# Kernel tuning notes

Measured on AMD Instinct MI355X. Metric: run time of the kernel, lower is better.

The kernel has to match this reference:

```python
import jax, jax.numpy as jnp
import numpy as np

T, IN, H, OUT = 4096, 512, 2048, 4


def setup_inputs() -> dict:
    key = jax.random.key(0)
    ks = jax.random.split(key, 10)
    s_in = 1.0 / np.sqrt(IN)   # fan-in scaled init for input weights
    s_h = 1.0 / np.sqrt(H)     # fan-in scaled init for recurrent weights
    return {
        "x": jax.random.normal(ks[0], (T, IN), jnp.float32),
        "h0": jnp.zeros((H,), jnp.float32),
        "hebb0": jnp.zeros((H, H), jnp.float32),
        "Wz": jax.random.normal(ks[1], (IN, H), jnp.float32) * s_in,
        "Uz": jax.random.normal(ks[2], (H, H), jnp.float32) * s_h,
        "bz": jnp.zeros((H,), jnp.float32),
        "Wr": jax.random.normal(ks[3], (IN, H), jnp.float32) * s_in,
        "Ur": jax.random.normal(ks[4], (H, H), jnp.float32) * s_h,
        "br": jnp.zeros((H,), jnp.float32),
        "Wh": jax.random.normal(ks[5], (IN, H), jnp.float32) * s_in,
        "Uh": jax.random.normal(ks[6], (H, H), jnp.float32) * s_h,
        "bh": jnp.zeros((H,), jnp.float32),
        "alpha": jax.random.normal(ks[7], (H, H), jnp.float32) * 0.01,
        "eta": jnp.full((1,), 0.01, jnp.float32),
        "Wo": jax.random.normal(ks[8], (H, OUT), jnp.float32) * s_h,
        "bo": jnp.zeros((OUT,), jnp.float32),
        "seed": 0,
    }


def reference(x, h0, hebb0, Wz, Uz, bz, Wr, Ur, br, Wh, Uh, bh, alpha, eta, Wo, bo, seed):
    eta_s = eta[0]
    # Precompute all input-to-hidden projections in one batched GEMM (time-parallel).
    xz = x @ Wz + bz          # [T, H]
    xr = x @ Wr + br          # [T, H]
    xh = x @ Wh + bh          # [T, H]

    def step(carry, xt):
        h, hebb = carry                         # h: [H], hebb: [H, H]
        xzt, xrt, xht = xt
        z = jax.nn.sigmoid(xzt + h @ Uz)        # update gate
        r = jax.nn.sigmoid(xrt + h @ Ur)        # reset gate
        rh = r * h
        # plastic recurrent weight: Uh + alpha (elementwise) * hebb fast weights
        h_tilde = jnp.tanh(xht + rh @ Uh + rh @ (alpha * hebb))
        h_new = (1.0 - z) * h + z * h_tilde
        # Hebbian trace: decaying outer-product of pre/post activities
        hebb_new = (1.0 - eta_s) * hebb + eta_s * jnp.outer(h, h_new)
        return (h_new, hebb_new), h_new

    (hT, hebbT), y = jax.lax.scan(step, (h0, hebb0), (xz, xr, xh))  # y: [T, H]
    output = y @ Wo + bo                         # [T, OUT]
    act_rng = jax.random.fold_in(jax.random.key(seed), 1)
    action = jax.random.categorical(act_rng, output[:, :2])  # [T]
    return (output, action, hT, hebbT)
```

## Files before the change

### kernel.cpp

```cpp
#include <hip/hip_runtime.h>
#include <stdint.h>

#define T_STEPS 4096
#define IN_DIM  512
#define H_DIM   2048
#define NBLK    256
#define STH     512

typedef unsigned int uint32;

__device__ __forceinline__ double wredd(double v) {
#pragma unroll
  for (int m = 32; m >= 1; m >>= 1) v += __shfl_xor(v, m, 64);
  return v;
}

__device__ __forceinline__ double agloadd(const double* p) {
  return __hip_atomic_load(const_cast<double*>(p), __ATOMIC_RELAXED, __HIP_MEMORY_SCOPE_AGENT);
}
__device__ __forceinline__ void agstored(double* p, double v) {
  __hip_atomic_store(p, v, __ATOMIC_RELAXED, __HIP_MEMORY_SCOPE_AGENT);
}

__device__ __forceinline__ void threefry2x32(uint32 k0, uint32 k1, uint32& x0, uint32& x1) {
  uint32 ks2 = k0 ^ k1 ^ 0x1BD11BDAu;
  x0 += k0; x1 += k1;
#define TF_R(r) { x0 += x1; x1 = (x1 << r) | (x1 >> (32 - r)); x1 ^= x0; }
  TF_R(13) TF_R(15) TF_R(26) TF_R(6)
  x0 += k1;  x1 += ks2 + 1u;
  TF_R(17) TF_R(29) TF_R(16) TF_R(24)
  x0 += ks2; x1 += k0 + 2u;
  TF_R(13) TF_R(15) TF_R(26) TF_R(6)
  x0 += k0;  x1 += k1 + 3u;
  TF_R(17) TF_R(29) TF_R(16) TF_R(24)
  x0 += k1;  x1 += ks2 + 4u;
  TF_R(13) TF_R(15) TF_R(26) TF_R(6)
  x0 += ks2; x1 += k0 + 5u;
#undef TF_R
}

__global__ void __launch_bounds__(256) transpose_all(
    const float* __restrict__ Uz, const float* __restrict__ Ur,
    const float* __restrict__ Uh, const float* __restrict__ Al,
    const float* __restrict__ Wz, const float* __restrict__ Wr, const float* __restrict__ Wh,
    const float* __restrict__ Hb0,
    float* __restrict__ UZT, float* __restrict__ URT,
    float* __restrict__ UHT, float* __restrict__ AT,
    float* __restrict__ WZT, float* __restrict__ WRT, float* __restrict__ WHT,
    float* __restrict__ HBT) {
  __shared__ float sm[64][65];
  const float* in; float* out; int R, C;
  switch (blockIdx.z) {
    case 0: in = Uz;  out = UZT; R = H_DIM; C = H_DIM; break;
    case 1: in = Ur;  out = URT; R = H_DIM; C = H_DIM; break;
    case 2: in = Uh;  out = UHT; R = H_DIM; C = H_DIM; break;
    case 3: in = Al;  out = AT;  R = H_DIM; C = H_DIM; break;
    case 4: in = Hb0; out = HBT; R = H_DIM; C = H_DIM; break;
    case 5: in = Wz;  out = WZT; R = IN_DIM; C = H_DIM; break;
    case 6: in = Wr;  out = WRT; R = IN_DIM; C = H_DIM; break;
    default: in = Wh; out = WHT; R = IN_DIM; C = H_DIM; break;
  }
  int r0 = blockIdx.y * 64, c0 = blockIdx.x * 64;
  if (r0 >= R) return;
#pragma unroll
  for (int l = 0; l < 16; ++l) {
    int idx = threadIdx.x + l * 256;
    int r = idx >> 6, c = idx & 63;
    sm[r][c] = in[(size_t)(r0 + r) * C + c0 + c];
  }
  __syncthreads();
#pragma unroll
  for (int l = 0; l < 16; ++l) {
    int idx = threadIdx.x + l * 256;
    int r = idx >> 6, c = idx & 63;
    out[(size_t)(c0 + r) * R + r0 + c] = sm[c][r];
  }
}

__device__ __forceinline__ void gridbar(uint32* slots, uint32* go, int b, int tid, uint32 phase) {
  __syncthreads();
  if (b == 0) {
    if (tid > 0 && tid < NBLK) {
      while (__hip_atomic_load(&slots[tid * 16], __ATOMIC_ACQUIRE, __HIP_MEMORY_SCOPE_AGENT) < phase) {}
    }
    __syncthreads();
    if (tid == 0) {
      __hip_atomic_store(go, phase, __ATOMIC_RELEASE, __HIP_MEMORY_SCOPE_AGENT);
    }
  } else {
    if (tid == 0) {
      __hip_atomic_store(&slots[b * 16], phase, __ATOMIC_RELEASE, __HIP_MEMORY_SCOPE_AGENT);
      while (__hip_atomic_load(go, __ATOMIC_ACQUIRE, __HIP_MEMORY_SCOPE_AGENT) < phase) {}
    }
  }
  __syncthreads();
}

__global__ void __launch_bounds__(STH, 1) scan_kernel(
    const float* __restrict__ h0, const float* __restrict__ x,
    const float* __restrict__ bz, const float* __restrict__ br, const float* __restrict__ bh,
    const float* __restrict__ eta_p,
    const float* __restrict__ UZT, const float* __restrict__ URT,
    const float* __restrict__ UHT, const float* __restrict__ AT,
    const float* __restrict__ WZT, const float* __restrict__ WRT, const float* __restrict__ WHT,
    float* __restrict__ HBT,
    double* __restrict__ Y, double* __restrict__ RH,
    uint32* slots, uint32* go) {
  __shared__ double hbufA[H_DIM];
  __shared__ double hbufB[H_DIM];
  __shared__ double rhsh[H_DIM];
  __shared__ float  xsh[IN_DIM];
  const int b = blockIdx.x, tid = threadIdx.x;
  const int w = tid >> 6, lane = tid & 63;
  const int j0 = b * 8, j = j0 + w;
  const double eta = (double)eta_p[0], dec = 1.0 - eta;
  const double bzj = (double)bz[j], brj = (double)br[j], bhj = (double)bh[j];

  double hb[32];
  const float* hbtj = HBT + (size_t)j * H_DIM;
#pragma unroll
  for (int m = 0; m < 32; ++m) hb[m] = (double)hbtj[m * 64 + lane];

  const float* uzp = UZT + (size_t)j * H_DIM;
  const float* urp = URT + (size_t)j * H_DIM;
  const float* uhp = UHT + (size_t)j * H_DIM;
  const float* atp = AT  + (size_t)j * H_DIM;
  const float* wzp = WZT + (size_t)j * IN_DIM;
  const float* wrp = WRT + (size_t)j * IN_DIM;
  const float* whp = WHT + (size_t)j * IN_DIM;
  double* hcur = hbufA; double* hprv = hbufB;
  uint32 phase = 0;

  for (int t = 0; t < T_STEPS; ++t) {
    if (t == 0) {
      for (int k = tid; k < H_DIM; k += STH) hcur[k] = (double)h0[k];
    } else {
      const double* yp = Y + (size_t)(t - 1) * H_DIM;
      for (int k = tid; k < H_DIM; k += STH) hcur[k] = agloadd(yp + k);
    }
    for (int k = tid; k < IN_DIM; k += STH) xsh[k] = x[(size_t)t * IN_DIM + k];
    __syncthreads();

    double sz = 0.0, sr = 0.0, sh = 0.0;
#pragma unroll
    for (int m = 0; m < IN_DIM / 64; ++m) {
      int i = m * 64 + lane;
      double xv = (double)xsh[i];
      sz = fma(xv, (double)wzp[i], sz);
      sr = fma(xv, (double)wrp[i], sr);
      sh = fma(xv, (double)whp[i], sh);
    }
#pragma unroll 8
    for (int m = 0; m < H_DIM / 64; ++m) {
      int i = m * 64 + lane;
      double hv = hcur[i];
      sz = fma(hv, (double)uzp[i], sz);
      sr = fma(hv, (double)urp[i], sr);
    }
    sz = wredd(sz); sr = wredd(sr);
    double z = 1.0 / (1.0 + exp(-(sz + bzj)));
    double r = 1.0 / (1.0 + exp(-(sr + brj)));
    double hj = hcur[j];
    if (lane == 0) agstored(&RH[j], r * hj);

    ++phase; gridbar(slots, go, b, tid, phase);

    for (int k = tid; k < H_DIM; k += STH) rhsh[k] = agloadd(&RH[k]);
    __syncthreads();

    double acc = sh;
    if (t == 0) {
#pragma unroll
      for (int m = 0; m < 32; ++m) {
        int i = m * 64 + lane;
        acc = fma(rhsh[i], fma((double)atp[i], hb[m], (double)uhp[i]), acc);
      }
    } else {
      double cj = eta * hj;
#pragma unroll
      for (int m = 0; m < 32; ++m) {
        int i = m * 64 + lane;
        double hbv = fma(cj, hprv[i], dec * hb[m]);
        hb[m] = hbv;
        acc = fma(rhsh[i], fma((double)atp[i], hbv, (double)uhp[i]), acc);
      }
    }
    acc = wredd(acc);
    double htl = tanh(acc + bhj);
    double hnew = (1.0 - z) * hj + z * htl;
    if (lane == 0) agstored(&Y[(size_t)t * H_DIM + j], hnew);

    ++phase; gridbar(slots, go, b, tid, phase);

    double* tmp = hcur; hcur = hprv; hprv = tmp;
  }

  const double* hA = Y + (size_t)(T_STEPS - 2) * H_DIM;
  double hbj = agloadd(Y + (size_t)(T_STEPS - 1) * H_DIM + j);
  float* hbto = HBT + (size_t)j * H_DIM;
#pragma unroll
  for (int m = 0; m < 32; ++m) {
    int i = m * 64 + lane;
    hbto[i] = (float)fma(eta * agloadd(hA + i), hbj, dec * hb[m]);
  }
}

__global__ void __launch_bounds__(64) outk(
    const double* __restrict__ Y, const float* __restrict__ Wo,
    const float* __restrict__ bo, const int* __restrict__ seedp,
    float* __restrict__ out) {
  int bid = blockIdx.x, lane = threadIdx.x;
  if (bid >= T_STEPS) {
    int jj = (bid - T_STEPS) * 64 + lane;
    out[20480 + jj] = (float)Y[(size_t)(T_STEPS - 1) * H_DIM + jj];
    return;
  }
  int t = bid;
  double a0 = 0., a1 = 0., a2 = 0., a3 = 0.;
  const double* yrow = Y + (size_t)t * H_DIM;
  for (int jj = lane; jj < H_DIM; jj += 64) {
    double yv = yrow[jj];
    float4 wv = ((const float4*)Wo)[jj];
    a0 = fma(yv, (double)wv.x, a0); a1 = fma(yv, (double)wv.y, a1);
    a2 = fma(yv, (double)wv.z, a2); a3 = fma(yv, (double)wv.w, a3);
  }
  a0 = wredd(a0); a1 = wredd(a1); a2 = wredd(a2); a3 = wredd(a3);
  if (lane == 0) {
    double l0 = a0 + (double)bo[0], l1 = a1 + (double)bo[1];
    double l2 = a2 + (double)bo[2], l3 = a3 + (double)bo[3];
    float4 o; o.x = (float)l0; o.y = (float)l1; o.z = (float)l2; o.w = (float)l3;
    ((float4*)out)[t] = o;

    long long sv = (long long)seedp[0];
    uint32 k0 = (uint32)(((unsigned long long)sv) >> 32), k1 = (uint32)(sv & 0xffffffffLL);
    uint32 ak0 = 0u, ak1 = 1u;
    threefry2x32(k0, k1, ak0, ak1);
    uint32 p0 = 0u, p1 = (uint32)(2 * t);
    threefry2x32(ak0, ak1, p0, p1);
    uint32 b0 = p0 ^ p1;
    uint32 q0 = 0u, q1 = (uint32)(2 * t + 1);
    threefry2x32(ak0, ak1, q0, q1);
    uint32 b1 = q0 ^ q1;
    const float tiny = 1.1754943508222875e-38f;
    float f0 = __uint_as_float((b0 >> 9) | 0x3f800000u) - 1.0f;
    float f1 = __uint_as_float((b1 >> 9) | 0x3f800000u) - 1.0f;
    float u0 = fmaxf(tiny, fmaf(f0, 1.0f - tiny, tiny));
    float u1 = fmaxf(tiny, fmaf(f1, 1.0f - tiny, tiny));
    float g0 = -logf(-logf(u0));
    float g1 = -logf(-logf(u1));
    double s0 = l0 + (double)g0, s1 = l1 + (double)g1;
    out[16384 + t] = (s1 > s0) ? 1.0f : 0.0f;
  }
}

__global__ void __launch_bounds__(256) hebbout_kernel(const float* __restrict__ HBT,
                                                      float* __restrict__ out) {
  __shared__ float sm[64][65];
  int j0 = blockIdx.x * 64, i0 = blockIdx.y * 64;
#pragma unroll
  for (int l = 0; l < 16; ++l) {
    int idx = threadIdx.x + l * 256;
    int r = idx >> 6, c = idx & 63;
    sm[r][c] = HBT[(size_t)(j0 + r) * H_DIM + i0 + c];
  }
  __syncthreads();
#pragma unroll
  for (int l = 0; l < 16; ++l) {
    int idx = threadIdx.x + l * 256;
    int r = idx >> 6, c = idx & 63;
    out[22528 + (size_t)(i0 + r) * H_DIM + j0 + c] = sm[c][r];
  }
}

extern "C" void kernel_launch(void* const* d_in, const int* in_sizes, int n_in,
                              void* d_out, int out_size, void* d_ws, size_t ws_size,
                              hipStream_t stream) {
  (void)in_sizes; (void)n_in; (void)out_size; (void)ws_size;
  const float* x     = (const float*)d_in[0];
  const float* h0    = (const float*)d_in[1];
  const float* hebb0 = (const float*)d_in[2];
  const float* Wz    = (const float*)d_in[3];
  const float* Uz    = (const float*)d_in[4];
  const float* bz    = (const float*)d_in[5];
  const float* Wr    = (const float*)d_in[6];
  const float* Ur    = (const float*)d_in[7];
  const float* br    = (const float*)d_in[8];
  const float* Wh    = (const float*)d_in[9];
  const float* Uh    = (const float*)d_in[10];
  const float* bh    = (const float*)d_in[11];
  const float* alpha = (const float*)d_in[12];
  const float* eta   = (const float*)d_in[13];
  const float* Wo    = (const float*)d_in[14];
  const float* bo    = (const float*)d_in[15];
  const int*   seed  = (const int*)d_in[16];

  const size_t TH = (size_t)T_STEPS * H_DIM;
  const size_t HH = (size_t)H_DIM * H_DIM;
  const size_t HI = (size_t)H_DIM * IN_DIM;
  double* Y  = (double*)d_ws;
  double* RH = Y + TH;
  float* UZT = (float*)(RH + H_DIM);
  float* URT = UZT + HH;
  float* UHT = URT + HH;
  float* AT  = UHT + HH;
  float* WZT = AT + HH;
  float* WRT = WZT + HI;
  float* WHT = WRT + HI;
  float* HBT = WHT + HI;
  uint32* slots = (uint32*)(HBT + HH);
  uint32* go    = slots + NBLK * 16;

  hipMemsetAsync(slots, 0, (NBLK * 16 + 16) * sizeof(uint32), stream);
  transpose_all<<<dim3(32, 32, 8), 256, 0, stream>>>(Uz, Ur, Uh, alpha, Wz, Wr, Wh, hebb0,
                                                     UZT, URT, UHT, AT, WZT, WRT, WHT, HBT);
  float* out = (float*)d_out;
  scan_kernel<<<NBLK, STH, 0, stream>>>(h0, x, bz, br, bh, eta,
                                        UZT, URT, UHT, AT, WZT, WRT, WHT,
                                        HBT, Y, RH, slots, go);
  outk<<<T_STEPS + 32, 64, 0, stream>>>(Y, Wo, bo, seed, out);
  hebbout_kernel<<<dim3(32, 32), 256, 0, stream>>>(HBT, out);
}
```

Measured before the change: 352.0 ms.

## Replicate broadcast buffers, per-block go flags, float4 loads, early hebb update

```diff
diff --git a/kernel.cpp b/kernel.cpp
--- a/kernel.cpp
+++ b/kernel.cpp
@@ -6,6 +6,7 @@
 #define H_DIM   2048
 #define NBLK    256
 #define STH     512
+#define NREP    8
 
 typedef unsigned int uint32;
 
@@ -77,20 +78,20 @@
   }
 }
 
-__device__ __forceinline__ void gridbar(uint32* slots, uint32* go, int b, int tid, uint32 phase) {
+__device__ __forceinline__ void gridbar(uint32* slots, uint32* goarr, int b, int tid, uint32 phase) {
   __syncthreads();
   if (b == 0) {
-    if (tid > 0 && tid < NBLK) {
+    if (tid >= 1 && tid < NBLK) {
       while (__hip_atomic_load(&slots[tid * 16], __ATOMIC_ACQUIRE, __HIP_MEMORY_SCOPE_AGENT) < phase) {}
     }
     __syncthreads();
-    if (tid == 0) {
-      __hip_atomic_store(go, phase, __ATOMIC_RELEASE, __HIP_MEMORY_SCOPE_AGENT);
+    if (tid < NBLK) {
+      __hip_atomic_store(&goarr[tid * 16], phase, __ATOMIC_RELEASE, __HIP_MEMORY_SCOPE_AGENT);
     }
   } else {
     if (tid == 0) {
       __hip_atomic_store(&slots[b * 16], phase, __ATOMIC_RELEASE, __HIP_MEMORY_SCOPE_AGENT);
-      while (__hip_atomic_load(go, __ATOMIC_ACQUIRE, __HIP_MEMORY_SCOPE_AGENT) < phase) {}
+      while (__hip_atomic_load(&goarr[b * 16], __ATOMIC_ACQUIRE, __HIP_MEMORY_SCOPE_AGENT) < phase) {}
     }
   }
   __syncthreads();
@@ -104,104 +105,124 @@
     const float* __restrict__ UHT, const float* __restrict__ AT,
     const float* __restrict__ WZT, const float* __restrict__ WRT, const float* __restrict__ WHT,
     float* __restrict__ HBT,
-    double* __restrict__ Y, double* __restrict__ RH,
-    uint32* slots, uint32* go) {
-  __shared__ double hbufA[H_DIM];
-  __shared__ double hbufB[H_DIM];
+    double* __restrict__ Y, double* __restrict__ Hrep, double* __restrict__ RHrep,
+    uint32* slots, uint32* goarr) {
+  __shared__ double hcur[H_DIM];
   __shared__ double rhsh[H_DIM];
   __shared__ float  xsh[IN_DIM];
   const int b = blockIdx.x, tid = threadIdx.x;
   const int w = tid >> 6, lane = tid & 63;
-  const int j0 = b * 8, j = j0 + w;
+  const int j = b * 8 + w;
+  const int rep = b & (NREP - 1);
   const double eta = (double)eta_p[0], dec = 1.0 - eta;
   const double bzj = (double)bz[j], brj = (double)br[j], bhj = (double)bh[j];
 
   double hb[32];
-  const float* hbtj = HBT + (size_t)j * H_DIM;
-#pragma unroll
-  for (int m = 0; m < 32; ++m) hb[m] = (double)hbtj[m * 64 + lane];
-
-  const float* uzp = UZT + (size_t)j * H_DIM;
-  const float* urp = URT + (size_t)j * H_DIM;
-  const float* uhp = UHT + (size_t)j * H_DIM;
-  const float* atp = AT  + (size_t)j * H_DIM;
-  const float* wzp = WZT + (size_t)j * IN_DIM;
-  const float* wrp = WRT + (size_t)j * IN_DIM;
-  const float* whp = WHT + (size_t)j * IN_DIM;
-  double* hcur = hbufA; double* hprv = hbufB;
+  const float4* hbt4 = (const float4*)(HBT + (size_t)j * H_DIM);
+#pragma unroll
+  for (int m = 0; m < 8; ++m) {
+    float4 v = hbt4[m * 64 + lane];
+    hb[4 * m + 0] = (double)v.x; hb[4 * m + 1] = (double)v.y;
+    hb[4 * m + 2] = (double)v.z; hb[4 * m + 3] = (double)v.w;
+  }
+
+  const float4* uz4 = (const float4*)(UZT + (size_t)j * H_DIM);
+  const float4* ur4 = (const float4*)(URT + (size_t)j * H_DIM);
+  const float4* uh4 = (const float4*)(UHT + (size_t)j * H_DIM);
+  const float4* at4 = (const float4*)(AT  + (size_t)j * H_DIM);
+  const float4* wz4 = (const float4*)(WZT + (size_t)j * IN_DIM);
+  const float4* wr4 = (const float4*)(WRT + (size_t)j * IN_DIM);
+  const float4* wh4 = (const float4*)(WHT + (size_t)j * IN_DIM);
   uint32 phase = 0;
 
   for (int t = 0; t < T_STEPS; ++t) {
     if (t == 0) {
       for (int k = tid; k < H_DIM; k += STH) hcur[k] = (double)h0[k];
     } else {
-      const double* yp = Y + (size_t)(t - 1) * H_DIM;
-      for (int k = tid; k < H_DIM; k += STH) hcur[k] = agloadd(yp + k);
+      const double* hp = Hrep + (size_t)rep * H_DIM;
+      for (int k = tid; k < H_DIM; k += STH) hcur[k] = agloadd(hp + k);
     }
     for (int k = tid; k < IN_DIM; k += STH) xsh[k] = x[(size_t)t * IN_DIM + k];
     __syncthreads();
 
     double sz = 0.0, sr = 0.0, sh = 0.0;
-#pragma unroll
-    for (int m = 0; m < IN_DIM / 64; ++m) {
-      int i = m * 64 + lane;
-      double xv = (double)xsh[i];
-      sz = fma(xv, (double)wzp[i], sz);
-      sr = fma(xv, (double)wrp[i], sr);
-      sh = fma(xv, (double)whp[i], sh);
-    }
-#pragma unroll 8
-    for (int m = 0; m < H_DIM / 64; ++m) {
-      int i = m * 64 + lane;
-      double hv = hcur[i];
-      sz = fma(hv, (double)uzp[i], sz);
-      sr = fma(hv, (double)urp[i], sr);
+    const float4* x4 = (const float4*)xsh;
+#pragma unroll
+    for (int m = 0; m < IN_DIM / 256; ++m) {
+      int i4 = m * 64 + lane;
+      float4 xv = x4[i4], az = wz4[i4], ar = wr4[i4], ah = wh4[i4];
+      sz = fma((double)xv.x, (double)az.x, sz); sz = fma((double)xv.y, (double)az.y, sz);
+      sz = fma((double)xv.z, (double)az.z, sz); sz = fma((double)xv.w, (double)az.w, sz);
+      sr = fma((double)xv.x, (double)ar.x, sr); sr = fma((double)xv.y, (double)ar.y, sr);
+      sr = fma((double)xv.z, (double)ar.z, sr); sr = fma((double)xv.w, (double)ar.w, sr);
+      sh = fma((double)xv.x, (double)ah.x, sh); sh = fma((double)xv.y, (double)ah.y, sh);
+      sh = fma((double)xv.z, (double)ah.z, sh); sh = fma((double)xv.w, (double)ah.w, sh);
+    }
+    const double2* h2 = (const double2*)hcur;
+#pragma unroll
+    for (int m = 0; m < H_DIM / 256; ++m) {
+      int i4 = m * 64 + lane;
+      float4 az = uz4[i4], ar = ur4[i4];
+      double2 hA = h2[2 * i4], hB = h2[2 * i4 + 1];
+      sz = fma(hA.x, (double)az.x, sz); sz = fma(hA.y, (double)az.y, sz);
+      sz = fma(hB.x, (double)az.z, sz); sz = fma(hB.y, (double)az.w, sz);
+      sr = fma(hA.x, (double)ar.x, sr); sr = fma(hA.y, (double)ar.y, sr);
+      sr = fma(hB.x, (double)ar.z, sr); sr = fma(hB.y, (double)ar.w, sr);
     }
     sz = wredd(sz); sr = wredd(sr);
     double z = 1.0 / (1.0 + exp(-(sz + bzj)));
     double r = 1.0 / (1.0 + exp(-(sr + brj)));
     double hj = hcur[j];
-    if (lane == 0) agstored(&RH[j], r * hj);
-
-    ++phase; gridbar(slots, go, b, tid, phase);
-
-    for (int k = tid; k < H_DIM; k += STH) rhsh[k] = agloadd(&RH[k]);
+    double rhj = r * hj;
+    if (lane < NREP) agstored(&RHrep[(size_t)lane * H_DIM + j], rhj);
+
+    ++phase; gridbar(slots, goarr, b, tid, phase);
+
+    {
+      const double* rp = RHrep + (size_t)rep * H_DIM;
+      for (int k = tid; k < H_DIM; k += STH) rhsh[k] = agloadd(rp + k);
+    }
     __syncthreads();
 
     double acc = sh;
-    if (t == 0) {
-#pragma unroll
-      for (int m = 0; m < 32; ++m) {
-        int i = m * 64 + lane;
-        acc = fma(rhsh[i], fma((double)atp[i], hb[m], (double)uhp[i]), acc);
-      }
-    } else {
-      double cj = eta * hj;
-#pragma unroll
-      for (int m = 0; m < 32; ++m) {
-        int i = m * 64 + lane;
-        double hbv = fma(cj, hprv[i], dec * hb[m]);
-        hb[m] = hbv;
-        acc = fma(rhsh[i], fma((double)atp[i], hbv, (double)uhp[i]), acc);
-      }
+    const double2* r2 = (const double2*)rhsh;
+#pragma unroll
+    for (int m = 0; m < 8; ++m) {
+      int i4 = m * 64 + lane;
+      float4 av = at4[i4], uv = uh4[i4];
+      double2 rA = r2[2 * i4], rB = r2[2 * i4 + 1];
+      acc = fma(rA.x, fma((double)av.x, hb[4 * m + 0], (double)uv.x), acc);
+      acc = fma(rA.y, fma((double)av.y, hb[4 * m + 1], (double)uv.y), acc);
+      acc = fma(rB.x, fma((double)av.z, hb[4 * m + 2], (double)uv.z), acc);
+      acc = fma(rB.y, fma((double)av.w, hb[4 * m + 3], (double)uv.w), acc);
     }
     acc = wredd(acc);
     double htl = tanh(acc + bhj);
     double hnew = (1.0 - z) * hj + z * htl;
-    if (lane == 0) agstored(&Y[(size_t)t * H_DIM + j], hnew);
-
-    ++phase; gridbar(slots, go, b, tid, phase);
-
-    double* tmp = hcur; hcur = hprv; hprv = tmp;
-  }
-
-  const double* hA = Y + (size_t)(T_STEPS - 2) * H_DIM;
-  double hbj = agloadd(Y + (size_t)(T_STEPS - 1) * H_DIM + j);
-  float* hbto = HBT + (size_t)j * H_DIM;
-#pragma unroll
-  for (int m = 0; m < 32; ++m) {
-    int i = m * 64 + lane;
-    hbto[i] = (float)fma(eta * agloadd(hA + i), hbj, dec * hb[m]);
+    if (lane < NREP) agstored(&Hrep[(size_t)lane * H_DIM + j], hnew);
+    if (lane == NREP) agstored(&Y[(size_t)t * H_DIM + j], hnew);
+
+    double cj = eta * hnew;
+#pragma unroll
+    for (int m = 0; m < 8; ++m) {
+      int i4 = m * 64 + lane;
+      double2 hA = h2[2 * i4], hB = h2[2 * i4 + 1];
+      hb[4 * m + 0] = fma(cj, hA.x, dec * hb[4 * m + 0]);
+      hb[4 * m + 1] = fma(cj, hA.y, dec * hb[4 * m + 1]);
+      hb[4 * m + 2] = fma(cj, hB.x, dec * hb[4 * m + 2]);
+      hb[4 * m + 3] = fma(cj, hB.y, dec * hb[4 * m + 3]);
+    }
+
+    ++phase; gridbar(slots, goarr, b, tid, phase);
+  }
+
+  float4* hbto4 = (float4*)(HBT + (size_t)j * H_DIM);
+#pragma unroll
+  for (int m = 0; m < 8; ++m) {
+    float4 o;
+    o.x = (float)hb[4 * m + 0]; o.y = (float)hb[4 * m + 1];
+    o.z = (float)hb[4 * m + 2]; o.w = (float)hb[4 * m + 3];
+    hbto4[m * 64 + lane] = o;
   }
 }
 
@@ -297,9 +318,10 @@
   const size_t TH = (size_t)T_STEPS * H_DIM;
   const size_t HH = (size_t)H_DIM * H_DIM;
   const size_t HI = (size_t)H_DIM * IN_DIM;
-  double* Y  = (double*)d_ws;
-  double* RH = Y + TH;
-  float* UZT = (float*)(RH + H_DIM);
+  double* Y     = (double*)d_ws;
+  double* Hrep  = Y + TH;
+  double* RHrep = Hrep + NREP * H_DIM;
+  float* UZT = (float*)(RHrep + NREP * H_DIM);
   float* URT = UZT + HH;
   float* UHT = URT + HH;
   float* AT  = UHT + HH;
@@ -308,15 +330,15 @@
   float* WHT = WRT + HI;
   float* HBT = WHT + HI;
   uint32* slots = (uint32*)(HBT + HH);
-  uint32* go    = slots + NBLK * 16;
-
-  hipMemsetAsync(slots, 0, (NBLK * 16 + 16) * sizeof(uint32), stream);
+  uint32* goarr = slots + NBLK * 16;
+
+  hipMemsetAsync(slots, 0, 2 * NBLK * 16 * sizeof(uint32), stream);
   transpose_all<<<dim3(32, 32, 8), 256, 0, stream>>>(Uz, Ur, Uh, alpha, Wz, Wr, Wh, hebb0,
                                                      UZT, URT, UHT, AT, WZT, WRT, WHT, HBT);
   float* out = (float*)d_out;
   scan_kernel<<<NBLK, STH, 0, stream>>>(h0, x, bz, br, bh, eta,
                                         UZT, URT, UHT, AT, WZT, WRT, WHT,
-                                        HBT, Y, RH, slots, go);
+                                        HBT, Y, Hrep, RHrep, slots, goarr);
   outk<<<T_STEPS + 32, 64, 0, stream>>>(Y, Wo, bo, seed, out);
   hebbout_kernel<<<dim3(32, 32), 256, 0, stream>>>(HBT, out);
 }
```

Result: slower. 403.7 ms (+14.7%).
